# Optimization experiments

Measured on AMD Instinct MI355X. Metric: run time of the kernel, lower is better.

## Reference

```python
import jax, jax.numpy as jnp
from jax import lax
import numpy as np

ARG_NAMES = ('x w1 b1 bn1_g bn1_b bn1_m bn1_v w2 b2 bn2_g bn2_b bn2_m bn2_v w3 b3 w4 b4 '
             'attn_w attn_b attn_u g0_w1 g0_b1 g0_w2 g0_b2 g1_w1 g1_b1 g1_w2 g1_b2 '
             'g2_w1 g2_b1 g2_w2 g2_b2 c_w1 c_b1 c_w2 c_b2 c_w3 c_b3 c_w4 c_b4').split()


def _conv1d(x, w, b, stride, pad):
    # x: [N, C, L], w: [O, I, K]
    y = lax.conv_general_dilated(x, w, (stride,), [(pad, pad)],
                                 dimension_numbers=('NCH', 'OIH', 'NCH'))
    return y + b[None, :, None]


def _bn(x, g, b, m, v, eps=1e-5):
    # eval-mode BatchNorm1d over channel dim of [N, C, L]
    inv = g / jnp.sqrt(v + eps)
    return (x - m[None, :, None]) * inv[None, :, None] + b[None, :, None]


def _forward(x, w1, b1, bn1_g, bn1_b, bn1_m, bn1_v, w2, b2, bn2_g, bn2_b, bn2_m, bn2_v,
             w3, b3, w4, b4, attn_w, attn_b, attn_u,
             g0_w1, g0_b1, g0_w2, g0_b2, g1_w1, g1_b1, g1_w2, g1_b2,
             g2_w1, g2_b1, g2_w2, g2_b2,
             c_w1, c_b1, c_w2, c_b2, c_w3, c_b3, c_w4, c_b4):
    B, S, C, T = x.shape  # [batch, crops, channels=64, time=400]
    h = x.reshape(-1, C, T)
    # CNN stack (dropout = identity in eval)
    h = _bn(jax.nn.elu(_conv1d(h, w1, b1, 2, 1)), bn1_g, bn1_b, bn1_m, bn1_v)   # [N,64,192]
    h = _bn(jax.nn.elu(_conv1d(h, w2, b2, 2, 0)), bn2_g, bn2_b, bn2_m, bn2_v)   # [N,64,87]
    h = jax.nn.elu(_conv1d(h, w3, b3, 1, 0))                                    # [N,64,82]
    h = lax.reduce_window(h, 0.0, lax.add, (1, 1, 3), (1, 1, 2), 'VALID') / 3.0  # [N,64,40]
    h = jax.nn.elu(_conv1d(h, w4, b4, 1, 0))                                    # [N,64,35]
    h = h.reshape(B, S, C, -1)  # [B, S, 64, 35]
    # Attention pooling over the crop dim (dim=1), sum=True
    v = jnp.tanh(jnp.einsum('bsch,hd->bscd', h, attn_w) + attn_b)
    alphas = jax.nn.softmax(jnp.einsum('bscd,d->bsc', v, attn_u), axis=1)
    h = jax.nn.elu((h * alphas[..., None]).sum(axis=1))  # [B, 64, 35]
    # GIN over complete 64-node graph (self-loops included, eps=0):
    # aggregation per node == sum over all nodes of the graph
    def gin(h, W1, B1, W2, B2):
        agg = h + h.sum(axis=1, keepdims=True)
        return jax.nn.relu(agg @ W1 + B1) @ W2 + B2
    h = jax.nn.relu(gin(h, g0_w1, g0_b1, g0_w2, g0_b2))
    h = jax.nn.relu(gin(h, g1_w1, g1_b1, g1_w2, g1_b2))
    h = gin(h, g2_w1, g2_b1, g2_w2, g2_b2)  # no act after last layer
    # Classifier
    f = h.reshape(B, -1)  # [B, 2240]
    f = jax.nn.elu(f @ c_w1 + c_b1)
    f = jax.nn.elu(f @ c_w2 + c_b2)
    f = jax.nn.elu(f @ c_w3 + c_b3)
    return f @ c_w4 + c_b4  # [B, 2]


def setup_inputs() -> dict:
    key = jax.random.key(0)
    ks = iter(jax.random.split(key, 64))
    def rn(shape, s=0.05):
        return jax.random.normal(next(ks), shape, dtype=jnp.float32) * s
    d = {}
    d['x'] = jax.random.normal(next(ks), (32, 16, 64, 400), dtype=jnp.float32)
    d['w1'] = rn((64, 64, 20)); d['b1'] = rn((64,))
    d['bn1_g'] = jnp.ones((64,), jnp.float32); d['bn1_b'] = jnp.zeros((64,), jnp.float32)
    d['bn1_m'] = jnp.zeros((64,), jnp.float32); d['bn1_v'] = jnp.ones((64,), jnp.float32)
    d['w2'] = rn((64, 64, 20)); d['b2'] = rn((64,))
    d['bn2_g'] = jnp.ones((64,), jnp.float32); d['bn2_b'] = jnp.zeros((64,), jnp.float32)
    d['bn2_m'] = jnp.zeros((64,), jnp.float32); d['bn2_v'] = jnp.ones((64,), jnp.float32)
    d['w3'] = rn((64, 64, 6)); d['b3'] = rn((64,))
    d['w4'] = rn((64, 64, 6)); d['b4'] = rn((64,))
    d['attn_w'] = rn((35, 256), 0.1); d['attn_b'] = rn((256,), 0.1); d['attn_u'] = rn((256,), 0.1)
    d['g0_w1'] = rn((35, 256)); d['g0_b1'] = rn((256,))
    d['g0_w2'] = rn((256, 256)); d['g0_b2'] = rn((256,))
    d['g1_w1'] = rn((256, 256)); d['g1_b1'] = rn((256,))
    d['g1_w2'] = rn((256, 256)); d['g1_b2'] = rn((256,))
    d['g2_w1'] = rn((256, 35)); d['g2_b1'] = rn((35,))
    d['g2_w2'] = rn((35, 35)); d['g2_b2'] = rn((35,))
    d['c_w1'] = rn((2240, 256)); d['c_b1'] = rn((256,))
    d['c_w2'] = rn((256, 64)); d['c_b2'] = rn((64,))
    d['c_w3'] = rn((64, 16)); d['c_b3'] = rn((16,))
    d['c_w4'] = rn((16, 2)); d['c_b4'] = rn((2,))
    return d


def reference(x, w1, b1, bn1_g, bn1_b, bn1_m, bn1_v, w2, b2, bn2_g, bn2_b, bn2_m, bn2_v,
              w3, b3, w4, b4, attn_w, attn_b, attn_u,
              g0_w1, g0_b1, g0_w2, g0_b2, g1_w1, g1_b1, g1_w2, g1_b2,
              g2_w1, g2_b1, g2_w2, g2_b2,
              c_w1, c_b1, c_w2, c_b2, c_w3, c_b3, c_w4, c_b4):
    return _forward(x, w1, b1, bn1_g, bn1_b, bn1_m, bn1_v, w2, b2, bn2_g, bn2_b, bn2_m, bn2_v,
                    w3, b3, w4, b4, attn_w, attn_b, attn_u,
                    g0_w1, g0_b1, g0_w2, g0_b2, g1_w1, g1_b1, g1_w2, g1_b2,
                    g2_w1, g2_b1, g2_w2, g2_b2,
                    c_w1, c_b1, c_w2, c_b2, c_w3, c_b3, c_w4, c_b4)
```

## Files before the change

kernel.cpp:

```cpp
#include <hip/hip_runtime.h>
#include <math.h>

typedef __attribute__((ext_vector_type(8))) __bf16 bf16x8;
typedef __attribute__((ext_vector_type(4))) __bf16 bf16x4;
typedef __attribute__((ext_vector_type(4))) float f32x4;

__device__ __forceinline__ float elu_f(float v) {
    return v > 0.f ? v : (expf(v) - 1.f);
}

__global__ __launch_bounds__(256) void prep_weights(
    const float* __restrict__ w1, const float* __restrict__ w2,
    const float* __restrict__ w3, const float* __restrict__ w4,
    __bf16* __restrict__ t1, __bf16* __restrict__ t2,
    __bf16* __restrict__ t3, __bf16* __restrict__ t4)
{
    int idx = blockIdx.x * 256 + threadIdx.x;
    if (idx < 81920) {
        int k = idx / 4096, r = idx - k * 4096, co = r >> 6, ci = r & 63;
        t1[idx] = (__bf16)w1[(co * 64 + ci) * 20 + k];
    } else if (idx < 163840) {
        int j = idx - 81920;
        int k = j / 4096, r = j - k * 4096, co = r >> 6, ci = r & 63;
        t2[j] = (__bf16)w2[(co * 64 + ci) * 20 + k];
    } else if (idx < 188416) {
        int j = idx - 163840;
        int k = j / 4096, r = j - k * 4096, co = r >> 6, ci = r & 63;
        t3[j] = (__bf16)w3[(co * 64 + ci) * 6 + k];
    } else if (idx < 212992) {
        int j = idx - 188416;
        int k = j / 4096, r = j - k * 4096, co = r >> 6, ci = r & 63;
        t4[j] = (__bf16)w4[(co * 64 + ci) * 6 + k];
    }
}

__global__ __launch_bounds__(256) void prep_tr(
    const float* __restrict__ g0w1, const float* __restrict__ g0w2,
    const float* __restrict__ g1w1, const float* __restrict__ g1w2,
    const float* __restrict__ g2w1, const float* __restrict__ g2w2,
    __bf16* __restrict__ d0, __bf16* __restrict__ d1, __bf16* __restrict__ d2,
    __bf16* __restrict__ d3, __bf16* __restrict__ d4, __bf16* __restrict__ d5)
{
    int bid = blockIdx.x;
    const float* src; __bf16* dst; int K, O, Kpad, Opad, tile;
    if (bid < 4)       { src = g0w1; dst = d0; K = 35;   O = 256; Kpad = 64;   Opad = 256; tile = bid; }
    else if (bid < 20) { src = g0w2; dst = d1; K = 256;  O = 256; Kpad = 256;  Opad = 256; tile = bid - 4; }
    else if (bid < 36) { src = g1w1; dst = d2; K = 256;  O = 256; Kpad = 256;  Opad = 256; tile = bid - 20; }
    else if (bid < 52) { src = g1w2; dst = d3; K = 256;  O = 256; Kpad = 256;  Opad = 256; tile = bid - 36; }
    else if (bid < 56) { src = g2w1; dst = d4; K = 256;  O = 35;  Kpad = 256;  Opad = 64;  tile = bid - 52; }
    else               { src = g2w2; dst = d5; K = 35;   O = 35;  Kpad = 64;   Opad = 64;  tile = 0; }
    int ktiles = Kpad >> 6;
    int ot = tile / ktiles, kt = tile - ot * ktiles;
    int k0 = kt * 64, o0 = ot * 64;
    size_t LOFF = (size_t)Opad * Kpad;
    __shared__ float tl[64][68];
    int c = threadIdx.x & 63, rr = threadIdx.x >> 6;
    #pragma unroll
    for (int it = 0; it < 16; ++it) {
        int r = rr + it * 4;
        int kk = k0 + r, oo = o0 + c;
        tl[r][c] = (kk < K && oo < O) ? src[(size_t)kk * O + oo] : 0.f;
    }
    __syncthreads();
    #pragma unroll
    for (int it = 0; it < 16; ++it) {
        int r = rr + it * 4;
        float v = tl[c][r];
        __bf16 hi = (__bf16)v;
        float lo = v - (float)hi;
        size_t pos = (size_t)(o0 + r) * Kpad + k0 + c;
        dst[pos] = hi;
        dst[LOFF + pos] = (__bf16)lo;
    }
}

template<int K, int STRIDE, int PAD, bool DO_BN, int IMODE,
         int NPB, int TPN, int LIN, int LOUT, int KCHUNK >
__global__ __launch_bounds__(NPB * TPN * 64, 2) void conv_mfma(
    const void* __restrict__ xin, const __bf16* __restrict__ wT,
    const float* __restrict__ bias,
    const float* __restrict__ bn_g, const float* __restrict__ bn_b,
    const float* __restrict__ bn_m, const float* __restrict__ bn_v,
    __bf16* __restrict__ y)
{
    constexpr int THREADS = NPB * TPN * 64;
    constexpr int TBLK  = TPN * 48;
    constexpr int VSPAN = STRIDE * (TBLK - 1) + K;
    constexpr int NBUF  = (STRIDE == 2) ? 2 : 1;
    constexpr int ROWS  = (VSPAN + NBUF - 1) / NBUF;
    __shared__ __align__(16) __bf16 sx[NPB * NBUF * ROWS * 72];
    __shared__ __align__(16) __bf16 sw[2 * 64 * 72];

    const int tid = threadIdx.x;
    const int nb  = blockIdx.x * NPB;

    if constexpr (IMODE == 0) {
        const float* xg = (const float*)xin + (size_t)nb * 64 * LIN;
        constexpr int NZROWS = PAD + (VSPAN - LIN - PAD);
        if (tid < NZROWS * 64) {
            int zr = tid >> 6;
            int v = (zr < PAD) ? zr : (LIN + PAD + zr - PAD);
            sx[((v & (NBUF - 1)) * ROWS + (v >> (NBUF - 1))) * 72 + (tid & 63)] = (__bf16)0.f;
        }
        constexpr int J4 = LIN / 4;
        constexpr int ITEMS = 16 * J4;
        constexpr int ITER = (ITEMS + THREADS - 1) / THREADS;
        #pragma unroll
        for (int it = 0; it < ITER; ++it) {
            int idx = it * THREADS + tid;
            if (ITEMS % THREADS == 0 || idx < ITEMS) {
                int jj = idx & 3;
                int g  = (idx >> 2) & 15;
                int q  = (idx >> 6) * 4 + jj;
                const float* xp = xg + (size_t)(4 * g) * LIN + 4 * q;
                float fa[4][4];
                #pragma unroll
                for (int u = 0; u < 4; ++u)
                    *(float4*)&fa[u][0] = *(const float4*)(xp + (size_t)u * LIN);
                #pragma unroll
                for (int e = 0; e < 4; ++e) {
                    int v = 4 * q + e + PAD;
                    bf16x4 wv = { (__bf16)fa[0][e], (__bf16)fa[1][e],
                                  (__bf16)fa[2][e], (__bf16)fa[3][e] };
                    *(bf16x4*)&sx[((v & (NBUF - 1)) * ROWS + (v >> (NBUF - 1))) * 72 + 4 * g] = wv;
                }
            }
        }
    }

    const int wave = tid >> 6, lane = tid & 63;
    const int n_l  = wave / TPN, tile = wave - n_l * TPN;
    const int m    = lane & 15, quad = lane >> 4;
    const __bf16* sxn = sx + (size_t)n_l * NBUF * ROWS * 72;

    f32x4 acc[3][4];
    #pragma unroll
    for (int mi = 0; mi < 3; ++mi)
        #pragma unroll
        for (int nj = 0; nj < 4; ++nj)
            acc[mi][nj] = (f32x4){0.f, 0.f, 0.f, 0.f};

    constexpr int WPT = (64 * 8) / THREADS;
    uint4 wreg[WPT];
    #pragma unroll
    for (int i = 0; i < WPT; ++i) {
        int idx = i * THREADS + tid;
        wreg[i] = *(const uint4*)(wT + (size_t)(idx >> 3) * 64 + (idx & 7) * 8);
    }
    #pragma unroll
    for (int i = 0; i < WPT; ++i) {
        int idx = i * THREADS + tid;
        *(uint4*)(sw + (size_t)(idx >> 3) * 72 + (idx & 7) * 8) = wreg[i];
    }
    __syncthreads();

    for (int kp = 0; kp < K; ++kp) {
        if (kp + 1 < K) {
            #pragma unroll
            for (int i = 0; i < WPT; ++i) {
                int idx = i * THREADS + tid;
                wreg[i] = *(const uint4*)(wT + (size_t)(kp + 1) * 4096 +
                                          (idx >> 3) * 64 + (idx & 7) * 8);
            }
        }
        const int xbuf   = (STRIDE == 2) ? (kp & 1) : 0;
        const int rowoff = (STRIDE == 2) ? (kp >> 1) : kp;
        const __bf16* abase = sxn + ((size_t)xbuf * ROWS + tile * 48 + m + rowoff) * 72;
        const __bf16* bbase = sw + (size_t)((kp & 1) * 64 + m) * 72;
        #pragma unroll
        for (int s = 0; s < 2; ++s) {
            bf16x8 af[3], bfr[4];
            #pragma unroll
            for (int mi = 0; mi < 3; ++mi)
                af[mi] = *(const bf16x8*)(abase + mi * (16 * 72) + s * 32 + quad * 8);
            #pragma unroll
            for (int nj = 0; nj < 4; ++nj)
                bfr[nj] = *(const bf16x8*)(bbase + nj * (16 * 72) + s * 32 + quad * 8);
            #pragma unroll
            for (int mi = 0; mi < 3; ++mi)
                #pragma unroll
                for (int nj = 0; nj < 4; ++nj)
                    acc[mi][nj] = __builtin_amdgcn_mfma_f32_16x16x32_bf16(
                        af[mi], bfr[nj], acc[mi][nj], 0, 0, 0);
        }
        if (kp + 1 < K) {
            __bf16* swd = sw + (size_t)((kp + 1) & 1) * 64 * 72;
            #pragma unroll
            for (int i = 0; i < WPT; ++i) {
                int idx = i * THREADS + tid;
                *(uint4*)(swd + (size_t)(idx >> 3) * 72 + (idx & 7) * 8) = wreg[i];
            }
        }
        __syncthreads();
    }

    #pragma unroll
    for (int nj = 0; nj < 4; ++nj) {
        const int co = nj * 16 + m;
        const float bi = bias[co];
        float scale = 1.f, shift = 0.f;
        if constexpr (DO_BN) {
            float inv = bn_g[co] / sqrtf(bn_v[co] + 1e-5f);
            scale = inv; shift = bn_b[co] - bn_m[co] * inv;
        }
        #pragma unroll
        for (int mi = 0; mi < 3; ++mi) {
            #pragma unroll
            for (int r = 0; r < 4; ++r) {
                int t = tile * 48 + mi * 16 + quad * 4 + r;
                if (t < LOUT) {
                    float v = acc[mi][nj][r] + bi;
                    v = elu_f(v);
                    if constexpr (DO_BN) v = v * scale + shift;
                    y[((size_t)(nb + n_l) * LOUT + t) * 64 + co] = (__bf16)v;
                }
            }
        }
    }
}

__global__ __launch_bounds__(128, 2) void conv234_fused(
    const __bf16* __restrict__ h1,
    const __bf16* __restrict__ wT2, const float* __restrict__ b2,
    const float* __restrict__ bn2g, const float* __restrict__ bn2b,
    const float* __restrict__ bn2m, const float* __restrict__ bn2v,
    const __bf16* __restrict__ wT3, const float* __restrict__ b3,
    const __bf16* __restrict__ wT4, const float* __restrict__ b4,
    __bf16* __restrict__ h4)
{
    __shared__ __align__(16) __bf16 bufA[2 * 96 * 72];
    __shared__ __align__(16) __bf16 bufB[87 * 72];
    __shared__ __align__(16) __bf16 sw[2 * 64 * 72];

    const int tid = threadIdx.x;
    const int n = blockIdx.x;
    const int wave = tid >> 6, lane = tid & 63;
    const int m = lane & 15, quad = lane >> 4;

    {
        const __bf16* src = h1 + (size_t)n * 192 * 64;
        #pragma unroll
        for (int it = 0; it < 12; ++it) {
            int idx = it * 128 + tid;
            int v = idx >> 3, c8 = (idx & 7) * 8;
            *(uint4*)(bufA + ((size_t)(v & 1) * 96 + (v >> 1)) * 72 + c8) =
                *(const uint4*)(src + (size_t)v * 64 + c8);
        }
    }
    __syncthreads();

    f32x4 acc[3][4];
    #pragma unroll
    for (int mi = 0; mi < 3; ++mi)
        #pragma unroll
        for (int nj = 0; nj < 4; ++nj)
            acc[mi][nj] = (f32x4){0.f, 0.f, 0.f, 0.f};

    for (int kb = 0; kb < 20; kb += 2) {
        if (kb) __syncthreads();
        #pragma unroll
        for (int it = 0; it < 8; ++it) {
            int idx = it * 128 + tid;
            int r = idx >> 3, p = idx & 7;
            *(uint4*)(sw + (size_t)r * 72 + p * 8) =
                *(const uint4*)(wT2 + (size_t)(kb + (r >> 6)) * 4096 + (r & 63) * 64 + p * 8);
        }
        __syncthreads();
        #pragma unroll
        for (int kp2 = 0; kp2 < 2; ++kp2) {
            const int kp = kb + kp2;
            const int buf = kp & 1, rowoff = kp >> 1;
            const int r0 = wave * 48 + m + rowoff;
            const __bf16* bbase = sw + (size_t)(kp2 * 64 + m) * 72;
            #pragma unroll
            for (int s = 0; s < 2; ++s) {
                bf16x8 af[3], bfr[4];
                #pragma unroll
                for (int mi = 0; mi < 3; ++mi) {
                    int rr = r0 + mi * 16; if (rr > 95) rr = 95;
                    af[mi] = *(const bf16x8*)(bufA + ((size_t)buf * 96 + rr) * 72 + s * 32 + quad * 8);
                }
                #pragma unroll
                for (int nj = 0; nj < 4; ++nj)
                    bfr[nj] = *(const bf16x8*)(bbase + nj * (16 * 72) + s * 32 + quad * 8);
                #pragma unroll
                for (int mi = 0; mi < 3; ++mi)
                    #pragma unroll
                    for (int nj = 0; nj < 4; ++nj)
                        acc[mi][nj] = __builtin_amdgcn_mfma_f32_16x16x32_bf16(
                            af[mi], bfr[nj], acc[mi][nj], 0, 0, 0);
            }
        }
    }
    __syncthreads();
    #pragma unroll
    for (int nj = 0; nj < 4; ++nj) {
        const int co = nj * 16 + m;
        const float bi = b2[co];
        float inv = bn2g[co] / sqrtf(bn2v[co] + 1e-5f);
        float shift = bn2b[co] - bn2m[co] * inv;
        #pragma unroll
        for (int mi = 0; mi < 3; ++mi)
            #pragma unroll
            for (int r = 0; r < 4; ++r) {
                int t = wave * 48 + mi * 16 + quad * 4 + r;
                if (t < 87) {
                    float v = elu_f(acc[mi][nj][r] + bi) * inv + shift;
                    bufB[t * 72 + co] = (__bf16)v;
                }
            }
    }
    __syncthreads();

    #pragma unroll
    for (int mi = 0; mi < 3; ++mi)
        #pragma unroll
        for (int nj = 0; nj < 4; ++nj)
            acc[mi][nj] = (f32x4){0.f, 0.f, 0.f, 0.f};

    for (int kb = 0; kb < 6; kb += 2) {
        if (kb) __syncthreads();
        #pragma unroll
        for (int it = 0; it < 8; ++it) {
            int idx = it * 128 + tid;
            int r = idx >> 3, p = idx & 7;
            *(uint4*)(sw + (size_t)r * 72 + p * 8) =
                *(const uint4*)(wT3 + (size_t)(kb + (r >> 6)) * 4096 + (r & 63) * 64 + p * 8);
        }
        __syncthreads();
        #pragma unroll
        for (int kp2 = 0; kp2 < 2; ++kp2) {
            const int kp = kb + kp2;
            const int r0 = wave * 48 + m + kp;
            const __bf16* bbase = sw + (size_t)(kp2 * 64 + m) * 72;
            #pragma unroll
            for (int s = 0; s < 2; ++s) {
                bf16x8 af[3], bfr[4];
                #pragma unroll
                for (int mi = 0; mi < 3; ++mi) {
                    int rr = r0 + mi * 16; if (rr > 86) rr = 86;
                    af[mi] = *(const bf16x8*)(bufB + (size_t)rr * 72 + s * 32 + quad * 8);
                }
                #pragma unroll
                for (int nj = 0; nj < 4; ++nj)
                    bfr[nj] = *(const bf16x8*)(bbase + nj * (16 * 72) + s * 32 + quad * 8);
                #pragma unroll
                for (int mi = 0; mi < 3; ++mi)
                    #pragma unroll
                    for (int nj = 0; nj < 4; ++nj)
                        acc[mi][nj] = __builtin_amdgcn_mfma_f32_16x16x32_bf16(
                            af[mi], bfr[nj], acc[mi][nj], 0, 0, 0);
            }
        }
    }
    __syncthreads();
    #pragma unroll
    for (int nj = 0; nj < 4; ++nj) {
        const int co = nj * 16 + m;
        const float bi = b3[co];
        #pragma unroll
        for (int mi = 0; mi < 3; ++mi)
            #pragma unroll
            for (int r = 0; r < 4; ++r) {
                int t = wave * 48 + mi * 16 + quad * 4 + r;
                if (t < 82)
                    bufA[t * 72 + co] = (__bf16)elu_f(acc[mi][nj][r] + bi);
            }
    }
    __syncthreads();

    #pragma unroll
    for (int it = 0; it < 20; ++it) {
        int idx = it * 128 + tid;
        int t = idx >> 6, co = idx & 63;
        float v = ((float)bufA[(2 * t) * 72 + co] + (float)bufA[(2 * t + 1) * 72 + co] +
                   (float)bufA[(2 * t + 2) * 72 + co]) * (1.f / 3.f);
        bufB[t * 72 + co] = (__bf16)v;
    }
    __syncthreads();

    f32x4 acc4[3][2];
    #pragma unroll
    for (int mi = 0; mi < 3; ++mi)
        #pragma unroll
        for (int nj = 0; nj < 2; ++nj)
            acc4[mi][nj] = (f32x4){0.f, 0.f, 0.f, 0.f};
    const int coh = wave * 32;

    for (int kb = 0; kb < 6; kb += 2) {
        if (kb) __syncthreads();
        #pragma unroll
        for (int it = 0; it < 8; ++it) {
            int idx = it * 128 + tid;
            int r = idx >> 3, p = idx & 7;
            *(uint4*)(sw + (size_t)r * 72 + p * 8) =
                *(const uint4*)(wT4 + (size_t)(kb + (r >> 6)) * 4096 + (r & 63) * 64 + p * 8);
        }
        __syncthreads();
        #pragma unroll
        for (int kp2 = 0; kp2 < 2; ++kp2) {
            const int kp = kb + kp2;
            const int r0 = m + kp;
            const __bf16* bbase = sw + (size_t)(kp2 * 64 + coh + m) * 72;
            #pragma unroll
            for (int s = 0; s < 2; ++s) {
                bf16x8 af[3], bfr[2];
                #pragma unroll
                for (int mi = 0; mi < 3; ++mi) {
                    int rr = r0 + mi * 16; if (rr > 39) rr = 39;
                    af[mi] = *(const bf16x8*)(bufB + (size_t)rr * 72 + s * 32 + quad * 8);
                }
                #pragma unroll
                for (int nj = 0; nj < 2; ++nj)
                    bfr[nj] = *(const bf16x8*)(bbase + nj * (16 * 72) + s * 32 + quad * 8);
                #pragma unroll
                for (int mi = 0; mi < 3; ++mi)
                    #pragma unroll
                    for (int nj = 0; nj < 2; ++nj)
                        acc4[mi][nj] = __builtin_amdgcn_mfma_f32_16x16x32_bf16(
                            af[mi], bfr[nj], acc4[mi][nj], 0, 0, 0);
            }
        }
    }
    #pragma unroll
    for (int nj = 0; nj < 2; ++nj) {
        const int co = coh + nj * 16 + m;
        const float bi = b4[co];
        #pragma unroll
        for (int mi = 0; mi < 3; ++mi)
            #pragma unroll
            for (int r = 0; r < 4; ++r) {
                int t = mi * 16 + quad * 4 + r;
                if (t < 35)
                    h4[((size_t)n * 35 + t) * 64 + co] = (__bf16)elu_f(acc4[mi][nj][r] + bi);
            }
    }
}

__global__ __launch_bounds__(256) void attn_pool_k(
    const __bf16* __restrict__ h, const float* __restrict__ W,
    const float* __restrict__ ab, const float* __restrict__ u,
    float* __restrict__ out)
{
    __shared__ float sW[35 * 256];
    __shared__ float sh[4][16 * 35 + 5];
    const int tid = threadIdx.x;
    const int pair0 = blockIdx.x * 4;
    for (int i = tid; i < 35 * 256; i += 256) sW[i] = W[i];
    for (int i = tid; i < 4 * 560; i += 256) {
        int q = i / 560, r = i - q * 560;
        int s = r / 35, t = r - s * 35;
        int bc = pair0 + q, b = bc >> 6, c = bc & 63;
        sh[q][s * 35 + t] = (float)h[(((size_t)b * 16 + s) * 35 + t) * 64 + c];
    }
    __syncthreads();

    const int wave = tid >> 6, lane = tid & 63;
    const int bc = pair0 + wave;
    const float* shw = sh[wave];

    float myu[4], myb[4];
    #pragma unroll
    for (int p = 0; p < 4; ++p) { myu[p] = u[lane + 64 * p]; myb[p] = ab[lane + 64 * p]; }

    float dot[16][4];
    #pragma unroll
    for (int s = 0; s < 16; ++s)
        #pragma unroll
        for (int p = 0; p < 4; ++p) dot[s][p] = myb[p];

    for (int t = 0; t < 35; ++t) {
        float w0 = sW[t * 256 + lane];
        float w1 = sW[t * 256 + lane + 64];
        float w2 = sW[t * 256 + lane + 128];
        float w3 = sW[t * 256 + lane + 192];
        #pragma unroll
        for (int s = 0; s < 16; ++s) {
            float hv = shw[s * 35 + t];
            dot[s][0] = fmaf(hv, w0, dot[s][0]);
            dot[s][1] = fmaf(hv, w1, dot[s][1]);
            dot[s][2] = fmaf(hv, w2, dot[s][2]);
            dot[s][3] = fmaf(hv, w3, dot[s][3]);
        }
    }

    float sc[16];
    #pragma unroll
    for (int s = 0; s < 16; ++s) {
        float v = tanhf(dot[s][0]) * myu[0] + tanhf(dot[s][1]) * myu[1]
                + tanhf(dot[s][2]) * myu[2] + tanhf(dot[s][3]) * myu[3];
        #pragma unroll
        for (int off = 1; off < 64; off <<= 1) v += __shfl_xor(v, off, 64);
        sc[s] = v;
    }

    float mx = sc[0];
    #pragma unroll
    for (int s = 1; s < 16; ++s) mx = fmaxf(mx, sc[s]);
    float e[16], sum = 0.f;
    #pragma unroll
    for (int s = 0; s < 16; ++s) { e[s] = expf(sc[s] - mx); sum += e[s]; }
    float inv = 1.f / sum;

    if (lane < 35) {
        float acc = 0.f;
        #pragma unroll
        for (int s = 0; s < 16; ++s) acc = fmaf(shw[s * 35 + lane], e[s] * inv, acc);
        out[(size_t)bc * 35 + lane] = elu_f(acc);
    }
}

#define APLANE (64 * 264)

__device__ __forceinline__ void gin_gemm_dev(
    const __bf16* As,
    const __bf16* __restrict__ Wg, int Kpad, int wlo, int Kout,
    const float* __restrict__ bias,
    int mode, __bf16* Ad, float* __restrict__ outg)
{
    const int lane = threadIdx.x & 63;
    const int wave = threadIdx.x >> 6;
    const int o0 = wave * 32;
    if (o0 >= ((Kout + 63) & ~63)) return;
    const int m = lane & 15, quad = lane >> 4;

    f32x4 acc[4][2];
    #pragma unroll
    for (int mi = 0; mi < 4; ++mi)
        #pragma unroll
        for (int nj = 0; nj < 2; ++nj)
            acc[mi][nj] = (f32x4){0.f, 0.f, 0.f, 0.f};

    for (int k0 = 0; k0 < Kpad; k0 += 32) {
        bf16x8 ah[4], al[4], bh[2], bl[2];
        #pragma unroll
        for (int mi = 0; mi < 4; ++mi) {
            const __bf16* ap = As + (size_t)(mi * 16 + m) * 264 + k0 + quad * 8;
            ah[mi] = *(const bf16x8*)ap;
            al[mi] = *(const bf16x8*)(ap + APLANE);
        }
        #pragma unroll
        for (int nj = 0; nj < 2; ++nj) {
            const __bf16* wp = Wg + (size_t)(o0 + nj * 16 + m) * Kpad + k0 + quad * 8;
            bh[nj] = *(const bf16x8*)wp;
            bl[nj] = *(const bf16x8*)(wp + wlo);
        }
        #pragma unroll
        for (int mi = 0; mi < 4; ++mi)
            #pragma unroll
            for (int nj = 0; nj < 2; ++nj) {
                acc[mi][nj] = __builtin_amdgcn_mfma_f32_16x16x32_bf16(
                    al[mi], bh[nj], acc[mi][nj], 0, 0, 0);
                acc[mi][nj] = __builtin_amdgcn_mfma_f32_16x16x32_bf16(
                    ah[mi], bl[nj], acc[mi][nj], 0, 0, 0);
                acc[mi][nj] = __builtin_amdgcn_mfma_f32_16x16x32_bf16(
                    ah[mi], bh[nj], acc[mi][nj], 0, 0, 0);
            }
    }

    #pragma unroll
    for (int nj = 0; nj < 2; ++nj) {
        const int o = o0 + nj * 16 + m;
        const bool ovalid = (o < Kout);
        const float bi = ovalid ? bias[o] : 0.f;
        float v[4][4];
        #pragma unroll
        for (int mi = 0; mi < 4; ++mi)
            #pragma unroll
            for (int r = 0; r < 4; ++r)
                v[mi][r] = acc[mi][nj][r] + bi;
        if (mode == 2) {
            if (ovalid) {
                #pragma unroll
                for (int mi = 0; mi < 4; ++mi)
                    #pragma unroll
                    for (int r = 0; r < 4; ++r)
                        outg[(size_t)(mi * 16 + quad * 4 + r) * Kout + o] = v[mi][r];
            }
        } else {
            float s = 0.f;
            #pragma unroll
            for (int mi = 0; mi < 4; ++mi)
                #pragma unroll
                for (int r = 0; r < 4; ++r) {
                    float rv = ovalid ? fmaxf(v[mi][r], 0.f) : 0.f;
                    v[mi][r] = rv;
                    s += rv;
                }
            if (mode == 1) {
                s += __shfl_xor(s, 16, 64);
                s += __shfl_xor(s, 32, 64);
            } else {
                s = 0.f;
            }
            #pragma unroll
            for (int mi = 0; mi < 4; ++mi)
                #pragma unroll
                for (int r = 0; r < 4; ++r) {
                    float a = v[mi][r] + s;
                    __bf16 hi = (__bf16)a;
                    size_t pos = (size_t)(mi * 16 + quad * 4 + r) * 264 + o;
                    Ad[pos] = hi;
                    Ad[APLANE + pos] = (__bf16)(a - (float)hi);
                }
        }
    }
}

__global__ __launch_bounds__(512) void gin_fused(
    const float* __restrict__ ha,
    const __bf16* __restrict__ gW0a, const __bf16* __restrict__ gW0b,
    const __bf16* __restrict__ gW1a, const __bf16* __restrict__ gW1b,
    const __bf16* __restrict__ gW2a, const __bf16* __restrict__ gW2b,
    const float* __restrict__ b0a, const float* __restrict__ b0b,
    const float* __restrict__ b1a, const float* __restrict__ b1b,
    const float* __restrict__ b2a, const float* __restrict__ b2b,
    float* __restrict__ H3)
{
    const int b = blockIdx.x, tid = threadIdx.x;
    __shared__ __align__(16) __bf16 sA[2][2 * APLANE];
    __shared__ float sS[64];
    const float* hab = ha + (size_t)b * 2240;

    if (tid < 64) {
        float s = 0.f;
        if (tid < 35)
            for (int n = 0; n < 64; ++n) s += hab[n * 35 + tid];
        sS[tid] = s;
    }
    __syncthreads();
    for (int idx = tid; idx < 64 * 64; idx += 512) {
        int n = idx >> 6, k = idx & 63;
        float a = (k < 35) ? hab[n * 35 + k] + sS[k] : 0.f;
        __bf16 hi = (__bf16)a;
        sA[0][n * 264 + k] = hi;
        sA[0][APLANE + n * 264 + k] = (__bf16)(a - (float)hi);
    }
    __syncthreads();

    gin_gemm_dev(sA[0], gW0a, 64,  16384, 256, b0a, 0, sA[1], nullptr); __syncthreads();
    gin_gemm_dev(sA[1], gW0b, 256, 65536, 256, b0b, 1, sA[0], nullptr); __syncthreads();
    gin_gemm_dev(sA[0], gW1a, 256, 65536, 256, b1a, 0, sA[1], nullptr); __syncthreads();
    gin_gemm_dev(sA[1], gW1b, 256, 65536, 256, b1b, 1, sA[0], nullptr); __syncthreads();
    gin_gemm_dev(sA[0], gW2a, 256, 16384, 35,  b2a, 0, sA[1], nullptr); __syncthreads();
    gin_gemm_dev(sA[1], gW2b, 64,  4096,  35,  b2b, 2, nullptr, H3 + (size_t)b * 2240);
}

__global__ __launch_bounds__(256) void cls1_part_k(
    const float* __restrict__ H3, const float* __restrict__ w1,
    float* __restrict__ s1p)
{
    const int b  = blockIdx.x;
    const int kc = blockIdx.y;
    const int k0 = kc * 140;
    __shared__ float sH[140];
    const int tid = threadIdx.x;
    if (tid < 140) sH[tid] = H3[(size_t)b * 2240 + k0 + tid];
    __syncthreads();
    const int o = (tid >> 6) * 64 + (tid & 63);
    float a0 = 0.f, a1 = 0.f, a2 = 0.f, a3 = 0.f;
    const float* wr = w1 + (size_t)k0 * 256 + o;
    #pragma unroll
    for (int k = 0; k < 140; k += 4) {
        a0 = fmaf(sH[k],     wr[(size_t)k * 256],       a0);
        a1 = fmaf(sH[k + 1], wr[(size_t)(k + 1) * 256], a1);
        a2 = fmaf(sH[k + 2], wr[(size_t)(k + 2) * 256], a2);
        a3 = fmaf(sH[k + 3], wr[(size_t)(k + 3) * 256], a3);
    }
    s1p[((size_t)kc * 32 + b) * 256 + o] = a0 + a1 + a2 + a3;
}

__global__ __launch_bounds__(256) void cls234_k(
    const float* __restrict__ s1p, const float* __restrict__ b1,
    const float* __restrict__ w2, const float* __restrict__ b2,
    const float* __restrict__ w3, const float* __restrict__ b3,
    const float* __restrict__ w4, const float* __restrict__ b4,
    float* __restrict__ out)
{
    const int b = blockIdx.x, tid = threadIdx.x;
    __shared__ float s1[256];
    __shared__ float part[4][64];
    __shared__ float s2[64];
    __shared__ float s3[16];
    {
        float acc = b1[tid];
        #pragma unroll
        for (int kc = 0; kc < 16; ++kc)
            acc += s1p[((size_t)kc * 32 + b) * 256 + tid];
        s1[tid] = elu_f(acc);
    }
    __syncthreads();
    {
        int kg = tid >> 6, o = tid & 63;
        float acc = 0.f;
        for (int k = kg * 64; k < kg * 64 + 64; ++k)
            acc = fmaf(s1[k], w2[k * 64 + o], acc);
        part[kg][o] = acc;
    }
    __syncthreads();
    if (tid < 64) {
        float acc = part[0][tid] + part[1][tid] + part[2][tid] + part[3][tid] + b2[tid];
        s2[tid] = elu_f(acc);
    }
    __syncthreads();
    if (tid < 16) {
        float acc = b3[tid];
        for (int k = 0; k < 64; ++k) acc = fmaf(s2[k], w3[k * 16 + tid], acc);
        s3[tid] = elu_f(acc);
    }
    __syncthreads();
    if (tid < 2) {
        float acc = b4[tid];
        for (int k = 0; k < 16; ++k) acc = fmaf(s3[k], w4[k * 2 + tid], acc);
        out[b * 2 + tid] = acc;
    }
}

extern "C" void kernel_launch(void* const* d_in, const int* in_sizes, int n_in,
                              void* d_out, int out_size, void* d_ws, size_t ws_size,
                              hipStream_t stream)
{
    const float* x     = (const float*)d_in[0];
    const float* w1    = (const float*)d_in[1];
    const float* b1    = (const float*)d_in[2];
    const float* bn1_g = (const float*)d_in[3];
    const float* bn1_b = (const float*)d_in[4];
    const float* bn1_m = (const float*)d_in[5];
    const float* bn1_v = (const float*)d_in[6];
    const float* w2    = (const float*)d_in[7];
    const float* b2    = (const float*)d_in[8];
    const float* bn2_g = (const float*)d_in[9];
    const float* bn2_b = (const float*)d_in[10];
    const float* bn2_m = (const float*)d_in[11];
    const float* bn2_v = (const float*)d_in[12];
    const float* w3    = (const float*)d_in[13];
    const float* b3    = (const float*)d_in[14];
    const float* w4    = (const float*)d_in[15];
    const float* b4    = (const float*)d_in[16];
    const float* attn_w = (const float*)d_in[17];
    const float* attn_b = (const float*)d_in[18];
    const float* attn_u = (const float*)d_in[19];
    const float* g0_w1 = (const float*)d_in[20];
    const float* g0_b1 = (const float*)d_in[21];
    const float* g0_w2 = (const float*)d_in[22];
    const float* g0_b2 = (const float*)d_in[23];
    const float* g1_w1 = (const float*)d_in[24];
    const float* g1_b1 = (const float*)d_in[25];
    const float* g1_w2 = (const float*)d_in[26];
    const float* g1_b2 = (const float*)d_in[27];
    const float* g2_w1 = (const float*)d_in[28];
    const float* g2_b1 = (const float*)d_in[29];
    const float* g2_w2 = (const float*)d_in[30];
    const float* g2_b2 = (const float*)d_in[31];
    const float* c_w1  = (const float*)d_in[32];
    const float* c_b1  = (const float*)d_in[33];
    const float* c_w2  = (const float*)d_in[34];
    const float* c_b2  = (const float*)d_in[35];
    const float* c_w3  = (const float*)d_in[36];
    const float* c_b3  = (const float*)d_in[37];
    const float* c_w4  = (const float*)d_in[38];
    const float* c_b4  = (const float*)d_in[39];
    float* out = (float*)d_out;

    char* ws = (char*)d_ws;
    __bf16* wT1  = (__bf16*)(ws + 0);
    __bf16* wT2  = (__bf16*)(ws + 163840);
    __bf16* wT3  = (__bf16*)(ws + 327680);
    __bf16* wT4  = (__bf16*)(ws + 376832);
    __bf16* h1   = (__bf16*)(ws + 425984);
    __bf16* h4   = (__bf16*)(ws + 13008896);
    float*  ha   = (float*)(ws + 15302656);
    __bf16* gW0a = (__bf16*)(ws + 15589376);
    __bf16* gW0b = (__bf16*)(ws + 15654912);
    __bf16* gW1a = (__bf16*)(ws + 15917056);
    __bf16* gW1b = (__bf16*)(ws + 16179200);
    __bf16* gW2a = (__bf16*)(ws + 16441344);
    __bf16* gW2b = (__bf16*)(ws + 16506880);
    float*  H3   = (float*)(ws + 16523264);
    float*  s1p  = (float*)(ws + 16809984);

    prep_weights<<<dim3(832), dim3(256), 0, stream>>>(w1, w2, w3, w4, wT1, wT2, wT3, wT4);
    prep_tr<<<dim3(57), dim3(256), 0, stream>>>(g0_w1, g0_w2, g1_w1, g1_w2, g2_w1, g2_w2,
                                                gW0a, gW0b, gW1a, gW1b, gW2a, gW2b);

    conv_mfma<20, 2, 1, true, 0, 1, 4, 400, 192, 2><<<dim3(512), dim3(256), 0, stream>>>(
        x, wT1, b1, bn1_g, bn1_b, bn1_m, bn1_v, h1);

    conv234_fused<<<dim3(512), dim3(128), 0, stream>>>(
        h1, wT2, b2, bn2_g, bn2_b, bn2_m, bn2_v, wT3, b3, wT4, b4, h4);

    attn_pool_k<<<dim3(512), dim3(256), 0, stream>>>(h4, attn_w, attn_b, attn_u, ha);

    gin_fused<<<dim3(32), dim3(512), 0, stream>>>(
        ha, gW0a, gW0b, gW1a, gW1b, gW2a, gW2b,
        g0_b1, g0_b2, g1_b1, g1_b2, g2_b1, g2_b2, H3);

    cls1_part_k<<<dim3(32, 16), dim3(256), 0, stream>>>(H3, c_w1, s1p);
    cls234_k<<<dim3(32), dim3(256), 0, stream>>>(s1p, c_b1, c_w2, c_b2, c_w3, c_b3,
                                                 c_w4, c_b4, out);
}
```

Measured before the change: 304.0 us.

## Load conv weights directly into registers and double wave count in fused conv

Both conv kernels stop staging weight tiles through shared memory. Each lane now loads its MFMA B fragments straight from global memory, prefetching the next tap into registers, which removes the per-tap __syncthreads barriers and LDS weight traffic. The fused conv2-4 kernel moves from 2 to 4 waves per block, splitting output channels between wave pairs and, for conv4, giving each wave 16 channels. The cost is redundant global or L2 weight reads across waves and more register pressure from the prefetch buffers.

```diff
diff --git a/kernel.cpp b/kernel.cpp
--- a/kernel.cpp
+++ b/kernel.cpp
@@ -89,7 +89,6 @@
     constexpr int NBUF  = (STRIDE == 2) ? 2 : 1;
     constexpr int ROWS  = (VSPAN + NBUF - 1) / NBUF;
     __shared__ __align__(16) __bf16 sx[NPB * NBUF * ROWS * 72];
-    __shared__ __align__(16) __bf16 sw[2 * 64 * 72];
 
     const int tid = threadIdx.x;
     const int nb  = blockIdx.x * NPB;
@@ -127,6 +126,7 @@
             }
         }
     }
+    __syncthreads();
 
     const int wave = tid >> 6, lane = tid & 63;
     const int n_l  = wave / TPN, tile = wave - n_l * TPN;
@@ -140,58 +140,44 @@
         for (int nj = 0; nj < 4; ++nj)
             acc[mi][nj] = (f32x4){0.f, 0.f, 0.f, 0.f};
 
-    constexpr int WPT = (64 * 8) / THREADS;
-    uint4 wreg[WPT];
-    #pragma unroll
-    for (int i = 0; i < WPT; ++i) {
-        int idx = i * THREADS + tid;
-        wreg[i] = *(const uint4*)(wT + (size_t)(idx >> 3) * 64 + (idx & 7) * 8);
-    }
-    #pragma unroll
-    for (int i = 0; i < WPT; ++i) {
-        int idx = i * THREADS + tid;
-        *(uint4*)(sw + (size_t)(idx >> 3) * 72 + (idx & 7) * 8) = wreg[i];
-    }
-    __syncthreads();
+    const __bf16* wbase = wT + (size_t)m * 64 + quad * 8;
+    bf16x8 bcur[2][4];
+    #pragma unroll
+    for (int s = 0; s < 2; ++s)
+        #pragma unroll
+        for (int nj = 0; nj < 4; ++nj)
+            bcur[s][nj] = *(const bf16x8*)(wbase + nj * (16 * 64) + s * 32);
 
     for (int kp = 0; kp < K; ++kp) {
-        if (kp + 1 < K) {
-            #pragma unroll
-            for (int i = 0; i < WPT; ++i) {
-                int idx = i * THREADS + tid;
-                wreg[i] = *(const uint4*)(wT + (size_t)(kp + 1) * 4096 +
-                                          (idx >> 3) * 64 + (idx & 7) * 8);
-            }
-        }
+        const int kn = (kp + 1 < K) ? kp + 1 : kp;
+        bf16x8 bnxt[2][4];
+        #pragma unroll
+        for (int s = 0; s < 2; ++s)
+            #pragma unroll
+            for (int nj = 0; nj < 4; ++nj)
+                bnxt[s][nj] = *(const bf16x8*)(wbase + (size_t)kn * 4096 + nj * (16 * 64) + s * 32);
+
         const int xbuf   = (STRIDE == 2) ? (kp & 1) : 0;
         const int rowoff = (STRIDE == 2) ? (kp >> 1) : kp;
         const __bf16* abase = sxn + ((size_t)xbuf * ROWS + tile * 48 + m + rowoff) * 72;
-        const __bf16* bbase = sw + (size_t)((kp & 1) * 64 + m) * 72;
         #pragma unroll
         for (int s = 0; s < 2; ++s) {
-            bf16x8 af[3], bfr[4];
+            bf16x8 af[3];
             #pragma unroll
             for (int mi = 0; mi < 3; ++mi)
                 af[mi] = *(const bf16x8*)(abase + mi * (16 * 72) + s * 32 + quad * 8);
             #pragma unroll
-            for (int nj = 0; nj < 4; ++nj)
-                bfr[nj] = *(const bf16x8*)(bbase + nj * (16 * 72) + s * 32 + quad * 8);
-            #pragma unroll
             for (int mi = 0; mi < 3; ++mi)
                 #pragma unroll
                 for (int nj = 0; nj < 4; ++nj)
                     acc[mi][nj] = __builtin_amdgcn_mfma_f32_16x16x32_bf16(
-                        af[mi], bfr[nj], acc[mi][nj], 0, 0, 0);
-        }
-        if (kp + 1 < K) {
-            __bf16* swd = sw + (size_t)((kp + 1) & 1) * 64 * 72;
-            #pragma unroll
-            for (int i = 0; i < WPT; ++i) {
-                int idx = i * THREADS + tid;
-                *(uint4*)(swd + (size_t)(idx >> 3) * 72 + (idx & 7) * 8) = wreg[i];
-            }
-        }
-        __syncthreads();
+                        af[mi], bcur[s][nj], acc[mi][nj], 0, 0, 0);
+        }
+        #pragma unroll
+        for (int s = 0; s < 2; ++s)
+            #pragma unroll
+            for (int nj = 0; nj < 4; ++nj)
+                bcur[s][nj] = bnxt[s][nj];
     }
 
     #pragma unroll
@@ -219,7 +205,7 @@
     }
 }
 
-__global__ __launch_bounds__(128, 2) void conv234_fused(
+__global__ __launch_bounds__(256, 2) void conv234_fused(
     const __bf16* __restrict__ h1,
     const __bf16* __restrict__ wT2, const float* __restrict__ b2,
     const float* __restrict__ bn2g, const float* __restrict__ bn2b,
@@ -230,18 +216,19 @@
 {
     __shared__ __align__(16) __bf16 bufA[2 * 96 * 72];
     __shared__ __align__(16) __bf16 bufB[87 * 72];
-    __shared__ __align__(16) __bf16 sw[2 * 64 * 72];
 
     const int tid = threadIdx.x;
     const int n = blockIdx.x;
     const int wave = tid >> 6, lane = tid & 63;
     const int m = lane & 15, quad = lane >> 4;
+    const int th = wave >> 1;
+    const int coh = (wave & 1) * 32;
 
     {
         const __bf16* src = h1 + (size_t)n * 192 * 64;
         #pragma unroll
-        for (int it = 0; it < 12; ++it) {
-            int idx = it * 128 + tid;
+        for (int it = 0; it < 6; ++it) {
+            int idx = it * 256 + tid;
             int v = idx >> 3, c8 = (idx & 7) * 8;
             *(uint4*)(bufA + ((size_t)(v & 1) * 96 + (v >> 1)) * 72 + c8) =
                 *(const uint4*)(src + (size_t)v * 64 + c8);
@@ -249,129 +236,143 @@
     }
     __syncthreads();
 
-    f32x4 acc[3][4];
-    #pragma unroll
-    for (int mi = 0; mi < 3; ++mi)
-        #pragma unroll
-        for (int nj = 0; nj < 4; ++nj)
-            acc[mi][nj] = (f32x4){0.f, 0.f, 0.f, 0.f};
-
-    for (int kb = 0; kb < 20; kb += 2) {
-        if (kb) __syncthreads();
-        #pragma unroll
-        for (int it = 0; it < 8; ++it) {
-            int idx = it * 128 + tid;
-            int r = idx >> 3, p = idx & 7;
-            *(uint4*)(sw + (size_t)r * 72 + p * 8) =
-                *(const uint4*)(wT2 + (size_t)(kb + (r >> 6)) * 4096 + (r & 63) * 64 + p * 8);
-        }
-        __syncthreads();
-        #pragma unroll
-        for (int kp2 = 0; kp2 < 2; ++kp2) {
-            const int kp = kb + kp2;
+    {
+        f32x4 acc[3][2];
+        #pragma unroll
+        for (int mi = 0; mi < 3; ++mi)
+            #pragma unroll
+            for (int nj = 0; nj < 2; ++nj)
+                acc[mi][nj] = (f32x4){0.f, 0.f, 0.f, 0.f};
+
+        const __bf16* wb = wT2 + (size_t)(coh + m) * 64 + quad * 8;
+        bf16x8 bcur[2][2];
+        #pragma unroll
+        for (int s = 0; s < 2; ++s)
+            #pragma unroll
+            for (int nj = 0; nj < 2; ++nj)
+                bcur[s][nj] = *(const bf16x8*)(wb + nj * (16 * 64) + s * 32);
+
+        for (int kp = 0; kp < 20; ++kp) {
+            const int kn = (kp + 1 < 20) ? kp + 1 : kp;
+            bf16x8 bnxt[2][2];
+            #pragma unroll
+            for (int s = 0; s < 2; ++s)
+                #pragma unroll
+                for (int nj = 0; nj < 2; ++nj)
+                    bnxt[s][nj] = *(const bf16x8*)(wb + (size_t)kn * 4096 + nj * (16 * 64) + s * 32);
+
             const int buf = kp & 1, rowoff = kp >> 1;
-            const int r0 = wave * 48 + m + rowoff;
-            const __bf16* bbase = sw + (size_t)(kp2 * 64 + m) * 72;
+            const int r0 = th * 48 + m + rowoff;
             #pragma unroll
             for (int s = 0; s < 2; ++s) {
-                bf16x8 af[3], bfr[4];
+                bf16x8 af[3];
                 #pragma unroll
                 for (int mi = 0; mi < 3; ++mi) {
                     int rr = r0 + mi * 16; if (rr > 95) rr = 95;
                     af[mi] = *(const bf16x8*)(bufA + ((size_t)buf * 96 + rr) * 72 + s * 32 + quad * 8);
                 }
                 #pragma unroll
-                for (int nj = 0; nj < 4; ++nj)
-                    bfr[nj] = *(const bf16x8*)(bbase + nj * (16 * 72) + s * 32 + quad * 8);
-                #pragma unroll
                 for (int mi = 0; mi < 3; ++mi)
                     #pragma unroll
-                    for (int nj = 0; nj < 4; ++nj)
+                    for (int nj = 0; nj < 2; ++nj)
                         acc[mi][nj] = __builtin_amdgcn_mfma_f32_16x16x32_bf16(
-                            af[mi], bfr[nj], acc[mi][nj], 0, 0, 0);
-            }
-        }
-    }
-    __syncthreads();
-    #pragma unroll
-    for (int nj = 0; nj < 4; ++nj) {
-        const int co = nj * 16 + m;
-        const float bi = b2[co];
-        float inv = bn2g[co] / sqrtf(bn2v[co] + 1e-5f);
-        float shift = bn2b[co] - bn2m[co] * inv;
+                            af[mi], bcur[s][nj], acc[mi][nj], 0, 0, 0);
+            }
+            #pragma unroll
+            for (int s = 0; s < 2; ++s)
+                #pragma unroll
+                for (int nj = 0; nj < 2; ++nj)
+                    bcur[s][nj] = bnxt[s][nj];
+        }
+
+        #pragma unroll
+        for (int nj = 0; nj < 2; ++nj) {
+            const int co = coh + nj * 16 + m;
+            const float bi = b2[co];
+            float inv = bn2g[co] / sqrtf(bn2v[co] + 1e-5f);
+            float shift = bn2b[co] - bn2m[co] * inv;
+            #pragma unroll
+            for (int mi = 0; mi < 3; ++mi)
+                #pragma unroll
+                for (int r = 0; r < 4; ++r) {
+                    int t = th * 48 + mi * 16 + quad * 4 + r;
+                    if (t < 87) {
+                        float v = elu_f(acc[mi][nj][r] + bi) * inv + shift;
+                        bufB[t * 72 + co] = (__bf16)v;
+                    }
+                }
+        }
+    }
+    __syncthreads();
+
+    {
+        f32x4 acc[3][2];
         #pragma unroll
         for (int mi = 0; mi < 3; ++mi)
             #pragma unroll
-            for (int r = 0; r < 4; ++r) {
-                int t = wave * 48 + mi * 16 + quad * 4 + r;
-                if (t < 87) {
-                    float v = elu_f(acc[mi][nj][r] + bi) * inv + shift;
-                    bufB[t * 72 + co] = (__bf16)v;
-                }
-            }
-    }
-    __syncthreads();
-
-    #pragma unroll
-    for (int mi = 0; mi < 3; ++mi)
-        #pragma unroll
-        for (int nj = 0; nj < 4; ++nj)
-            acc[mi][nj] = (f32x4){0.f, 0.f, 0.f, 0.f};
-
-    for (int kb = 0; kb < 6; kb += 2) {
-        if (kb) __syncthreads();
-        #pragma unroll
-        for (int it = 0; it < 8; ++it) {
-            int idx = it * 128 + tid;
-            int r = idx >> 3, p = idx & 7;
-            *(uint4*)(sw + (size_t)r * 72 + p * 8) =
-                *(const uint4*)(wT3 + (size_t)(kb + (r >> 6)) * 4096 + (r & 63) * 64 + p * 8);
-        }
-        __syncthreads();
-        #pragma unroll
-        for (int kp2 = 0; kp2 < 2; ++kp2) {
-            const int kp = kb + kp2;
-            const int r0 = wave * 48 + m + kp;
-            const __bf16* bbase = sw + (size_t)(kp2 * 64 + m) * 72;
+            for (int nj = 0; nj < 2; ++nj)
+                acc[mi][nj] = (f32x4){0.f, 0.f, 0.f, 0.f};
+
+        const __bf16* wb = wT3 + (size_t)(coh + m) * 64 + quad * 8;
+        bf16x8 bcur[2][2];
+        #pragma unroll
+        for (int s = 0; s < 2; ++s)
+            #pragma unroll
+            for (int nj = 0; nj < 2; ++nj)
+                bcur[s][nj] = *(const bf16x8*)(wb + nj * (16 * 64) + s * 32);
+
+        #pragma unroll
+        for (int kp = 0; kp < 6; ++kp) {
+            const int kn = (kp + 1 < 6) ? kp + 1 : kp;
+            bf16x8 bnxt[2][2];
+            #pragma unroll
+            for (int s = 0; s < 2; ++s)
+                #pragma unroll
+                for (int nj = 0; nj < 2; ++nj)
+                    bnxt[s][nj] = *(const bf16x8*)(wb + (size_t)kn * 4096 + nj * (16 * 64) + s * 32);
+
+            const int r0 = th * 48 + m + kp;
             #pragma unroll
             for (int s = 0; s < 2; ++s) {
-                bf16x8 af[3], bfr[4];
+                bf16x8 af[3];
                 #pragma unroll
                 for (int mi = 0; mi < 3; ++mi) {
                     int rr = r0 + mi * 16; if (rr > 86) rr = 86;
                     af[mi] = *(const bf16x8*)(bufB + (size_t)rr * 72 + s * 32 + quad * 8);
                 }
                 #pragma unroll
-                for (int nj = 0; nj < 4; ++nj)
-                    bfr[nj] = *(const bf16x8*)(bbase + nj * (16 * 72) + s * 32 + quad * 8);
-                #pragma unroll
                 for (int mi = 0; mi < 3; ++mi)
                     #pragma unroll
-                    for (int nj = 0; nj < 4; ++nj)
+                    for (int nj = 0; nj < 2; ++nj)
                         acc[mi][nj] = __builtin_amdgcn_mfma_f32_16x16x32_bf16(
-                            af[mi], bfr[nj], acc[mi][nj], 0, 0, 0);
-            }
-        }
-    }
-    __syncthreads();
-    #pragma unroll
-    for (int nj = 0; nj < 4; ++nj) {
-        const int co = nj * 16 + m;
-        const float bi = b3[co];
-        #pragma unroll
-        for (int mi = 0; mi < 3; ++mi)
-            #pragma unroll
-            for (int r = 0; r < 4; ++r) {
-                int t = wave * 48 + mi * 16 + quad * 4 + r;
-                if (t < 82)
-                    bufA[t * 72 + co] = (__bf16)elu_f(acc[mi][nj][r] + bi);
-            }
-    }
-    __syncthreads();
-
-    #pragma unroll
-    for (int it = 0; it < 20; ++it) {
-        int idx = it * 128 + tid;
+                            af[mi], bcur[s][nj], acc[mi][nj], 0, 0, 0);
+            }
+            #pragma unroll
+            for (int s = 0; s < 2; ++s)
+                #pragma unroll
+                for (int nj = 0; nj < 2; ++nj)
+                    bcur[s][nj] = bnxt[s][nj];
+        }
+
+        #pragma unroll
+        for (int nj = 0; nj < 2; ++nj) {
+            const int co = coh + nj * 16 + m;
+            const float bi = b3[co];
+            #pragma unroll
+            for (int mi = 0; mi < 3; ++mi)
+                #pragma unroll
+                for (int r = 0; r < 4; ++r) {
+                    int t = th * 48 + mi * 16 + quad * 4 + r;
+                    if (t < 82)
+                        bufA[t * 72 + co] = (__bf16)elu_f(acc[mi][nj][r] + bi);
+                }
+        }
+    }
+    __syncthreads();
+
+    #pragma unroll
+    for (int it = 0; it < 10; ++it) {
+        int idx = it * 256 + tid;
         int t = idx >> 6, co = idx & 63;
         float v = ((float)bufA[(2 * t) * 72 + co] + (float)bufA[(2 * t + 1) * 72 + co] +
                    (float)bufA[(2 * t + 2) * 72 + co]) * (1.f / 3.f);
@@ -379,52 +380,47 @@
     }
     __syncthreads();
 
-    f32x4 acc4[3][2];
-    #pragma unroll
-    for (int mi = 0; mi < 3; ++mi)
-        #pragma unroll
-        for (int nj = 0; nj < 2; ++nj)
-            acc4[mi][nj] = (f32x4){0.f, 0.f, 0.f, 0.f};
-    const int coh = wave * 32;
-
-    for (int kb = 0; kb < 6; kb += 2) {
-        if (kb) __syncthreads();
-        #pragma unroll
-        for (int it = 0; it < 8; ++it) {
-            int idx = it * 128 + tid;
-            int r = idx >> 3, p = idx & 7;
-            *(uint4*)(sw + (size_t)r * 72 + p * 8) =
-                *(const uint4*)(wT4 + (size_t)(kb + (r >> 6)) * 4096 + (r & 63) * 64 + p * 8);
-        }
-        __syncthreads();
-        #pragma unroll
-        for (int kp2 = 0; kp2 < 2; ++kp2) {
-            const int kp = kb + kp2;
+    {
+        const int co0 = wave * 16;
+        f32x4 acc4[3];
+        #pragma unroll
+        for (int mi = 0; mi < 3; ++mi)
+            acc4[mi] = (f32x4){0.f, 0.f, 0.f, 0.f};
+
+        const __bf16* wb = wT4 + (size_t)(co0 + m) * 64 + quad * 8;
+        bf16x8 bcur[2];
+        #pragma unroll
+        for (int s = 0; s < 2; ++s)
+            bcur[s] = *(const bf16x8*)(wb + s * 32);
+
+        #pragma unroll
+        for (int kp = 0; kp < 6; ++kp) {
+            const int kn = (kp + 1 < 6) ? kp + 1 : kp;
+            bf16x8 bnxt[2];
+            #pragma unroll
+            for (int s = 0; s < 2; ++s)
+                bnxt[s] = *(const bf16x8*)(wb + (size_t)kn * 4096 + s * 32);
+
             const int r0 = m + kp;
-            const __bf16* bbase = sw + (size_t)(kp2 * 64 + coh + m) * 72;
             #pragma unroll
             for (int s = 0; s < 2; ++s) {
-                bf16x8 af[3], bfr[2];
+                bf16x8 af[3];
                 #pragma unroll
                 for (int mi = 0; mi < 3; ++mi) {
                     int rr = r0 + mi * 16; if (rr > 39) rr = 39;
                     af[mi] = *(const bf16x8*)(bufB + (size_t)rr * 72 + s * 32 + quad * 8);
                 }
                 #pragma unroll
-                for (int nj = 0; nj < 2; ++nj)
-                    bfr[nj] = *(const bf16x8*)(bbase + nj * (16 * 72) + s * 32 + quad * 8);
-                #pragma unroll
                 for (int mi = 0; mi < 3; ++mi)
-                    #pragma unroll
-                    for (int nj = 0; nj < 2; ++nj)
-                        acc4[mi][nj] = __builtin_amdgcn_mfma_f32_16x16x32_bf16(
-                            af[mi], bfr[nj], acc4[mi][nj], 0, 0, 0);
-            }
-        }
-    }
-    #pragma unroll
-    for (int nj = 0; nj < 2; ++nj) {
-        const int co = coh + nj * 16 + m;
+                    acc4[mi] = __builtin_amdgcn_mfma_f32_16x16x32_bf16(
+                        af[mi], bcur[s], acc4[mi], 0, 0, 0);
+            }
+            #pragma unroll
+            for (int s = 0; s < 2; ++s)
+                bcur[s] = bnxt[s];
+        }
+
+        const int co = co0 + m;
         const float bi = b4[co];
         #pragma unroll
         for (int mi = 0; mi < 3; ++mi)
@@ -432,7 +428,7 @@
             for (int r = 0; r < 4; ++r) {
                 int t = mi * 16 + quad * 4 + r;
                 if (t < 35)
-                    h4[((size_t)n * 35 + t) * 64 + co] = (__bf16)elu_f(acc4[mi][nj][r] + bi);
+                    h4[((size_t)n * 35 + t) * 64 + co] = (__bf16)elu_f(acc4[mi][r] + bi);
             }
     }
 }
@@ -786,7 +782,7 @@
     conv_mfma<20, 2, 1, true, 0, 1, 4, 400, 192, 2><<<dim3(512), dim3(256), 0, stream>>>(
         x, wT1, b1, bn1_g, bn1_b, bn1_m, bn1_v, h1);
 
-    conv234_fused<<<dim3(512), dim3(128), 0, stream>>>(
+    conv234_fused<<<dim3(512), dim3(256), 0, stream>>>(
         h1, wT2, b2, bn2_g, bn2_b, bn2_m, bn2_v, wT3, b3, wT4, b4, h4);
 
     attn_pool_k<<<dim3(512), dim3(256), 0, stream>>>(h4, attn_w, attn_b, attn_u, ha);
```

Result: slower. 326.7 us (+7.5%).
